# Optimization experiments

Measured on AMD Instinct MI355X. Metric: run time of the kernel, lower is better.

## Reference

```python
import jax, jax.numpy as jnp
import numpy as np

E, D, H, B = 8, 64, 512, 32768  # n_experts, state_dim, hidden width, batch
IN = D + 3  # x, t, sin(omega*t), cos(omega*t)


def setup_inputs() -> dict:
    key = jax.random.key(0)
    ks = jax.random.split(key, 12)
    s = 0.02
    return {
        "t": jax.random.uniform(ks[0], (1,), dtype=jnp.float32),
        "x": jax.random.normal(ks[1], (B, D), dtype=jnp.float32),
        "expert_weights": jax.random.uniform(ks[2], (B, E), dtype=jnp.float32),
        "omega": jnp.arange(1, E + 1, dtype=jnp.float32),  # omega_i = i+1
        "W1": jax.random.normal(ks[3], (E, H, IN), dtype=jnp.float32) * s,
        "b1": jnp.zeros((E, H), dtype=jnp.float32),
        "W2": jax.random.normal(ks[4], (E, H, H), dtype=jnp.float32) * s,
        "b2": jnp.zeros((E, H), dtype=jnp.float32),
        "W3": jax.random.normal(ks[5], (E, H, H), dtype=jnp.float32) * s,
        "b3": jnp.zeros((E, H), dtype=jnp.float32),
        "W4": jax.random.normal(ks[6], (E, D, H), dtype=jnp.float32) * s,
        "b4": jnp.zeros((E, D), dtype=jnp.float32),
    }


def reference(t, x, expert_weights, omega, W1, b1, W2, b2, W3, b3, W4, b4):
    # Dense path of ExpertODEEnsemble.forward: all experts active.
    nB = x.shape[0]
    tb = jnp.broadcast_to(t, (nB,))                       # (B,)
    wt = omega[:, None] * tb[None, :]                     # (E, B)
    # Per-expert inputs: [x, t, sin(wt), cos(wt)] -> (E, B, D+3)
    xe = jnp.broadcast_to(x[None], (E, nB, D))
    te = jnp.broadcast_to(tb[None, :, None], (E, nB, 1))
    inp = jnp.concatenate([xe, te, jnp.sin(wt)[..., None], jnp.cos(wt)[..., None]], axis=-1)
    h = jnp.tanh(jnp.einsum('ebi,ehi->ebh', inp, W1) + b1[:, None, :])
    h = jnp.tanh(jnp.einsum('ebh,egh->ebg', h, W2) + b2[:, None, :])
    h = jnp.tanh(jnp.einsum('ebh,egh->ebg', h, W3) + b3[:, None, :])
    dyn = jnp.einsum('ebh,edh->ebd', h, W4) + b4[:, None, :]   # (E, B, D)
    # Weighted combine: sum_e w[b,e] * dyn[e,b,:]
    dx_dt = jnp.einsum('be,ebd->bd', expert_weights, dyn)
    return dx_dt
```

## Files before the change

kernel.cpp:

```cpp
#include <hip/hip_runtime.h>
#include <hip/hip_bf16.h>


typedef unsigned short ushort_t;
typedef unsigned int u32;
typedef unsigned long long u64;
typedef __attribute__((ext_vector_type(8))) short short8;
typedef __attribute__((ext_vector_type(4))) float floatx4;
typedef __attribute__((ext_vector_type(16))) float floatx16;
typedef __attribute__((ext_vector_type(4))) int intx4;

#define W1A_OFF 0u
#define W2A_OFF 524288u
#define W3A_OFF 4718592u
#define W4A_OFF 8912896u
#define XB_OFF  9437184u
#define B1E_OFF 13631488u

#define X_OFF_L 135168
#define SYNC_OFF 152064
#define SMEM_SZ 152128

static __device__ __forceinline__ u32 pk2bf(float a, float b) {
  union { __hip_bfloat162 h; u32 u; } v;
  v.h = __float22bfloat162_rn(make_float2(a, b));
  return v.u;
}

static __device__ __forceinline__ float pade_tanh(float x) {
  float x2 = x * x;
  float num = __builtin_fmaf(x2, __builtin_fmaf(x2, 1.0f, 105.0f), 945.0f);
  float den = __builtin_fmaf(x2, __builtin_fmaf(x2, 15.0f, 420.0f), 945.0f);
  return x * num * __builtin_amdgcn_rcpf(den);
}

static __device__ __forceinline__ void ald16(const void* g, void* l) {
  __builtin_amdgcn_global_load_lds((__attribute__((address_space(1))) void*)g,
                                   (__attribute__((address_space(3))) void*)l,
                                   16, 0, 0);
}

static __device__ __forceinline__ floatx16 mfma32(short8 a, short8 b, floatx16 c) {
  return __builtin_amdgcn_mfma_f32_32x32x16_bf16(a, b, c, 0, 0, 0);
}

static __device__ __forceinline__ void waitge(const int* p, int tgt) {
  while (*(volatile const int*)p < tgt) __builtin_amdgcn_s_sleep(1);
  __asm__ __volatile__("" ::: "memory");
}

static __device__ __forceinline__ void bump(int* p, int lane) {
  __asm__ __volatile__("s_waitcnt lgkmcnt(0)" ::: "memory");
  if (lane == 0) atomicAdd(p, 1);
}

__global__ __launch_bounds__(256) void prep_kernel(
    const float* __restrict__ t, const float* __restrict__ x,
    const float* __restrict__ omega, const float* __restrict__ W1,
    const float* __restrict__ b1, const float* __restrict__ W2,
    const float* __restrict__ W3, const float* __restrict__ W4,
    char* __restrict__ ws) {
  int i = blockIdx.x * 256 + threadIdx.x;
  if (i < 32768) {
    int e = i >> 12, rem = i & 4095, outr = rem >> 3, kg = rem & 7;
    int lane = (outr & 31) | ((kg & 1) << 5);
    int w = outr >> 6, ol = (outr >> 5) & 1, kc = kg >> 1;
    int dest = e * 4096 + ((w * 4 + kc) * 2 + ol) * 64 + lane;
    const float* s = W1 + (e * 512 + outr) * 67 + kg * 8;
    ((intx4*)(ws + W1A_OFF))[dest] = (intx4){
        (int)pk2bf(s[0], s[1]), (int)pk2bf(s[2], s[3]),
        (int)pk2bf(s[4], s[5]), (int)pk2bf(s[6], s[7])};
    return;
  }
  i -= 32768;
  if (i < 262144) {
    int e = i >> 15, rem = i & 32767, outr = rem >> 6, kg = rem & 63;
    int lane = (outr & 31) | ((kg & 1) << 5);
    int w = outr >> 6, ol = (outr >> 5) & 1, kc = kg >> 1;
    int dest = e * 32768 + ((w * 32 + kc) * 2 + ol) * 64 + lane;
    const floatx4* s = (const floatx4*)(W2 + ((e << 9) + outr) * 512 + (kg << 3));
    floatx4 lo = s[0], hi = s[1];
    ((intx4*)(ws + W2A_OFF))[dest] = (intx4){
        (int)pk2bf(lo[0], lo[1]), (int)pk2bf(lo[2], lo[3]),
        (int)pk2bf(hi[0], hi[1]), (int)pk2bf(hi[2], hi[3])};
    return;
  }
  i -= 262144;
  if (i < 262144) {
    int e = i >> 15, rem = i & 32767, outr = rem >> 6, kg = rem & 63;
    int lane = (outr & 31) | ((kg & 1) << 5);
    int w = outr >> 6, ol = (outr >> 5) & 1, kc = kg >> 1;
    int dest = e * 32768 + ((w * 32 + kc) * 2 + ol) * 64 + lane;
    const floatx4* s = (const floatx4*)(W3 + ((e << 9) + outr) * 512 + (kg << 3));
    floatx4 lo = s[0], hi = s[1];
    ((intx4*)(ws + W3A_OFF))[dest] = (intx4){
        (int)pk2bf(lo[0], lo[1]), (int)pk2bf(lo[2], lo[3]),
        (int)pk2bf(hi[0], hi[1]), (int)pk2bf(hi[2], hi[3])};
    return;
  }
  i -= 262144;
  if (i < 32768) {
    int e = i >> 12, rem = i & 4095, outr = rem >> 6, kg = rem & 63;
    int lane = (outr & 31) | ((kg & 1) << 5);
    int o4 = outr >> 5, kc = kg >> 1;
    int dest = e * 4096 + (o4 * 32 + kc) * 64 + lane;
    const floatx4* s = (const floatx4*)(W4 + ((e << 6) + outr) * 512 + (kg << 3));
    floatx4 lo = s[0], hi = s[1];
    ((intx4*)(ws + W4A_OFF))[dest] = (intx4){
        (int)pk2bf(lo[0], lo[1]), (int)pk2bf(lo[2], lo[3]),
        (int)pk2bf(hi[0], hi[1]), (int)pk2bf(hi[2], hi[3])};
    return;
  }
  i -= 32768;
  if (i < 262144) {
    const floatx4* s = (const floatx4*)(x + i * 8);
    floatx4 lo = s[0], hi = s[1];
    ((intx4*)(ws + XB_OFF))[i] = (intx4){
        (int)pk2bf(lo[0], lo[1]), (int)pk2bf(lo[2], lo[3]),
        (int)pk2bf(hi[0], hi[1]), (int)pk2bf(hi[2], hi[3])};
    return;
  }
  i -= 262144;
  if (i < 4096) {
    float tv = t[0];
    int e = i >> 9;
    float om = omega[e];
    ((float*)(ws + B1E_OFF))[i] = b1[i] + tv * W1[i * 67 + 64]
        + sinf(om * tv) * W1[i * 67 + 65] + cosf(om * tv) * W1[i * 67 + 66];
  }
}


template <int NKC, bool ISX>
static __device__ __forceinline__ void mlp_layer(
    const char* __restrict__ bsrc, char* __restrict__ act,
    int* kcp, int* pub, int lane, int w, int q1, int r31,
    const char* __restrict__ Abase, const float* __restrict__ bias,
    int pub_tgt, int tgt_cov, int tgt_oth, int khm, bool do_epi_wait) {
  const int voff = lane * 16;
  const char* sp = Abase + w * (NKC * 2048) + voff;

  floatx16 acc[2][4];
#pragma unroll
  for (int ol = 0; ol < 2; ++ol) {
    int fe0 = w * 64 + ol * 32 + 4 * q1;
#pragma unroll
    for (int g = 0; g < 4; ++g) {
      floatx4 bv = *(const floatx4*)(bias + fe0 + 8 * g);
#pragma unroll
      for (int nt = 0; nt < 4; ++nt) {
        acc[ol][nt][4 * g + 0] = bv[0];
        acc[ol][nt][4 * g + 1] = bv[1];
        acc[ol][nt][4 * g + 2] = bv[2];
        acc[ol][nt][4 * g + 3] = bv[3];
      }
    }
  }
  short8 a0 = *(const short8*)(sp);
  short8 a1 = *(const short8*)(sp + 1024);
  sp += 2048;

  const int NG = NKC / 4;
#pragma unroll 1
  for (int g = 0; g < NG; ++g) {
    if (!ISX) waitge(pub + g, pub_tgt);
    const char* gb = bsrc + g * (4 * 4224) + voff;
    short8 b0 = *(const short8*)(gb);
    short8 b1v = *(const short8*)(gb + 1024);
    short8 b2 = *(const short8*)(gb + 2048);
    short8 b3 = *(const short8*)(gb + 3072);
#pragma unroll
    for (int j = 0; j < 4; ++j) {
      short8 an0 = *(const short8*)(sp);
      short8 an1 = *(const short8*)(sp + 1024);
      sp += 2048;
      const char* bn = gb + ((j + 1) & 3) * 4224;
      short8 bn0 = *(const short8*)(bn);
      short8 bn1 = *(const short8*)(bn + 1024);
      short8 bn2 = *(const short8*)(bn + 2048);
      short8 bn3 = *(const short8*)(bn + 3072);
      acc[0][0] = mfma32(a0, b0, acc[0][0]);
      acc[0][1] = mfma32(a0, b1v, acc[0][1]);
      acc[0][2] = mfma32(a0, b2, acc[0][2]);
      acc[0][3] = mfma32(a0, b3, acc[0][3]);
      acc[1][0] = mfma32(a1, b0, acc[1][0]);
      acc[1][1] = mfma32(a1, b1v, acc[1][1]);
      acc[1][2] = mfma32(a1, b2, acc[1][2]);
      acc[1][3] = mfma32(a1, b3, acc[1][3]);
      a0 = an0; a1 = an1;
      b0 = bn0; b1v = bn1; b2 = bn2; b3 = bn3;
    }
    bump(kcp + w, lane);
  }

  if (do_epi_wait) {
    for (int w2 = 0; w2 < 8; ++w2)
      waitge(kcp + w2, ((w2 >> 2) == khm) ? tgt_cov : tgt_oth);
  }
#pragma unroll
  for (int ol = 0; ol < 2; ++ol) {
#pragma unroll
    for (int g = 0; g < 4; ++g) {
      int ko = ol * 4 + g;
      char* base = act + (4 * w + (ko >> 1)) * 4224
                   + (((ko & 1) * 32 + r31) << 4) + q1 * 8;
#pragma unroll
      for (int nt = 0; nt < 4; ++nt) {
        float v0 = pade_tanh(acc[ol][nt][4 * g + 0]);
        float v1 = pade_tanh(acc[ol][nt][4 * g + 1]);
        float v2 = pade_tanh(acc[ol][nt][4 * g + 2]);
        float v3 = pade_tanh(acc[ol][nt][4 * g + 3]);
        u32 lo = pk2bf(v0, v1), hi = pk2bf(v2, v3);
        *(u64*)(base + nt * 1024) = ((u64)hi << 32) | lo;
      }
    }
  }
  bump(pub + w, lane);
}

extern "C" __global__ __launch_bounds__(512) void fused_kernel(
    const char* __restrict__ ws, const float* __restrict__ b2,
    const float* __restrict__ b3, const float* __restrict__ b4,
    const float* __restrict__ ew, float* __restrict__ out) {
  extern __shared__ char smem[];
  char* act = smem;
  char* xreg = smem + X_OFF_L;
  int* kcp = (int*)(smem + SYNC_OFF);
  int* pub = kcp + 8;

  const int t = threadIdx.x, lane = t & 63, w = t >> 6;
  const int q1 = lane >> 5, r31 = lane & 31;
  const int row0 = blockIdx.x << 7;
  const int voff = lane * 16;

  if (t < 16) ((int*)(smem + SYNC_OFF))[t] = 0;

  const ushort_t* xb = (const ushort_t*)(ws + XB_OFF);
#pragma unroll
  for (int s = 0; s < 2; ++s) {
    int u = w + 8 * s, v = u >> 2, nt = u & 3;
    ald16(xb + (row0 + nt * 32 + r31) * 64 + (2 * v + q1) * 8,
          xreg + v * 4224 + nt * 1024);
  }
  __syncthreads();

  const int rt = w & 3, kh = w >> 2;
  const int row_l4 = row0 + rt * 32 + r31;
  floatx16 oacc[2] = {};

  for (int e = 0; e < 8; ++e) {
    mlp_layer<4, true>(xreg, act, kcp, pub, lane, w, q1, r31,
                       ws + W1A_OFF + e * 65536,
                       (const float*)(ws + B1E_OFF) + e * 512,
                       0, 21 * e + (w & 3) - 3, 21 * e + w - 11, w >> 2, e > 0);
    mlp_layer<32, false>(act, act, kcp, pub, lane, w, q1, r31,
                         ws + W2A_OFF + e * 524288, b2 + e * 512,
                         3 * e + 1, 21 * e + w + 2, 21 * e + w + 2, 0, true);
    mlp_layer<32, false>(act, act, kcp, pub, lane, w, q1, r31,
                         ws + W3A_OFF + e * 524288, b3 + e * 512,
                         3 * e + 2, 21 * e + w + 10, 21 * e + w + 10, 0, true);

    {
      const char* spA = ws + W4A_OFF + e * 65536 + voff;
      const float sc = ew[row_l4 * 8 + e];
      floatx16 acc4[2] = {};
      int kc0 = kh * 16;
      short8 a0 = *(const short8*)(spA + kc0 * 1024);
      short8 a1 = *(const short8*)(spA + 32768 + kc0 * 1024);
#pragma unroll 1
      for (int gl = 0; gl < 4; ++gl) {
        int g = kh * 4 + gl;
        waitge(pub + g, 3 * e + 3);
        const char* gb = act + g * (4 * 4224) + rt * 1024 + voff;
        short8 b = *(const short8*)(gb);
#pragma unroll
        for (int j = 0; j < 4; ++j) {
          int kc = g * 4 + j;
          short8 an0 = *(const short8*)(spA + (kc + 1) * 1024);
          short8 an1 = *(const short8*)(spA + 32768 + (kc + 1) * 1024);
          short8 bn = *(const short8*)(gb + ((j + 1) & 3) * 4224);
          acc4[0] = mfma32(a0, b, acc4[0]);
          acc4[1] = mfma32(a1, b, acc4[1]);
          a0 = an0; a1 = an1; b = bn;
        }
        bump(kcp + w, lane);
      }
      if (kh == 0) {
        const float* bp = b4 + e * 64;
#pragma unroll
        for (int ol = 0; ol < 2; ++ol) {
          int fe0 = ol * 32 + 4 * q1;
#pragma unroll
          for (int g = 0; g < 4; ++g) {
            floatx4 bv = *(const floatx4*)(bp + fe0 + 8 * g);
            oacc[ol][4 * g + 0] += sc * (acc4[ol][4 * g + 0] + bv[0]);
            oacc[ol][4 * g + 1] += sc * (acc4[ol][4 * g + 1] + bv[1]);
            oacc[ol][4 * g + 2] += sc * (acc4[ol][4 * g + 2] + bv[2]);
            oacc[ol][4 * g + 3] += sc * (acc4[ol][4 * g + 3] + bv[3]);
          }
        }
      } else {
#pragma unroll
        for (int ol = 0; ol < 2; ++ol)
#pragma unroll
          for (int i = 0; i < 16; ++i) oacc[ol][i] += sc * acc4[ol][i];
      }
    }
  }

  __syncthreads();
  if (kh == 1) {
#pragma unroll
    for (int ol = 0; ol < 2; ++ol)
#pragma unroll
      for (int g = 0; g < 4; ++g) {
        floatx4 p = {oacc[ol][4 * g + 0], oacc[ol][4 * g + 1],
                     oacc[ol][4 * g + 2], oacc[ol][4 * g + 3]};
        *(floatx4*)(act + rt * 8192 + ol * 4096 + g * 1024 + lane * 16) = p;
      }
  }
  __syncthreads();
  if (kh == 0) {
    float* orow = out + row_l4 * 64;
#pragma unroll
    for (int ol = 0; ol < 2; ++ol)
#pragma unroll
      for (int g = 0; g < 4; ++g) {
        floatx4 p = *(const floatx4*)(act + rt * 8192 + ol * 4096 + g * 1024 + lane * 16);
        floatx4 v = {oacc[ol][4 * g + 0] + p[0], oacc[ol][4 * g + 1] + p[1],
                     oacc[ol][4 * g + 2] + p[2], oacc[ol][4 * g + 3] + p[3]};
        *(floatx4*)(orow + ol * 32 + 8 * g + 4 * q1) = v;
      }
  }
}

extern "C" void kernel_launch(void* const* d_in, const int* in_sizes, int n_in,
                              void* d_out, int out_size, void* d_ws, size_t ws_size,
                              hipStream_t stream) {
  const float* t  = (const float*)d_in[0];
  const float* x  = (const float*)d_in[1];
  const float* ew = (const float*)d_in[2];
  const float* om = (const float*)d_in[3];
  const float* W1 = (const float*)d_in[4];
  const float* b1 = (const float*)d_in[5];
  const float* W2 = (const float*)d_in[6];
  const float* b2 = (const float*)d_in[7];
  const float* W3 = (const float*)d_in[8];
  const float* b3 = (const float*)d_in[9];
  const float* W4 = (const float*)d_in[10];
  const float* b4 = (const float*)d_in[11];
  char* ws = (char*)d_ws;
  float* out = (float*)d_out;
  (void)in_sizes; (void)n_in; (void)ws_size; (void)out_size;

  static int smem_set = 0;
  if (!smem_set) {
    hipFuncSetAttribute((const void*)fused_kernel,
                        hipFuncAttributeMaxDynamicSharedMemorySize, SMEM_SZ);
    smem_set = 1;
  }
  prep_kernel<<<3344, 256, 0, stream>>>(t, x, om, W1, b1, W2, W3, W4, ws);
  fused_kernel<<<256, 512, SMEM_SZ, stream>>>(ws, b2, b3, b4, ew, out);
}
```

Measured before the change: 441.3 us.

## Rotate per-wave K-group order to stagger LDS access and flag waits

Each wave now starts its K-group loop at an offset based on its wave index and wraps around. This applies to the hidden layers and the output layer. The aim is to spread LDS bank and flag-polling contention across waves and let waves start on groups that are already published. The epilogue wait targets are recomputed as a common base plus a per-wave stagger to match the new completion order. The risk is that mismatched counter targets cause races or over-waiting.

```diff
diff --git a/kernel.cpp b/kernel.cpp
--- a/kernel.cpp
+++ b/kernel.cpp
@@ -136,9 +136,10 @@
     const char* __restrict__ bsrc, char* __restrict__ act,
     int* kcp, int* pub, int lane, int w, int q1, int r31,
     const char* __restrict__ Abase, const float* __restrict__ bias,
-    int pub_tgt, int tgt_cov, int tgt_oth, int khm, bool do_epi_wait) {
+    int pub_tgt, int epi_base, bool epi_stagger, bool do_epi_wait) {
   const int voff = lane * 16;
-  const char* sp = Abase + w * (NKC * 2048) + voff;
+  const char* Aw = Abase + w * (NKC * 2048) + voff;
+  const int NG = NKC / 4;
 
   floatx16 acc[2][4];
 #pragma unroll
@@ -156,24 +157,26 @@
       }
     }
   }
-  short8 a0 = *(const short8*)(sp);
-  short8 a1 = *(const short8*)(sp + 1024);
-  sp += 2048;
-
-  const int NG = NKC / 4;
+  const int g0 = w & (NG - 1);
+  short8 a0 = *(const short8*)(Aw + g0 * 8192);
+  short8 a1 = *(const short8*)(Aw + g0 * 8192 + 1024);
+
 #pragma unroll 1
-  for (int g = 0; g < NG; ++g) {
+  for (int gi = 0; gi < NG; ++gi) {
+    const int g = (w + gi) & (NG - 1);
     if (!ISX) waitge(pub + g, pub_tgt);
     const char* gb = bsrc + g * (4 * 4224) + voff;
     short8 b0 = *(const short8*)(gb);
     short8 b1v = *(const short8*)(gb + 1024);
     short8 b2 = *(const short8*)(gb + 2048);
     short8 b3 = *(const short8*)(gb + 3072);
+    const char* Ag = Aw + g * 8192;
+    const char* An = Aw + (((w + gi + 1) & (NG - 1)) * 8192);
 #pragma unroll
     for (int j = 0; j < 4; ++j) {
-      short8 an0 = *(const short8*)(sp);
-      short8 an1 = *(const short8*)(sp + 1024);
-      sp += 2048;
+      const char* ap = (j < 3) ? (Ag + (j + 1) * 2048) : An;
+      short8 an0 = *(const short8*)(ap);
+      short8 an1 = *(const short8*)(ap + 1024);
       const char* bn = gb + ((j + 1) & 3) * 4224;
       short8 bn0 = *(const short8*)(bn);
       short8 bn1 = *(const short8*)(bn + 1024);
@@ -194,8 +197,12 @@
   }
 
   if (do_epi_wait) {
-    for (int w2 = 0; w2 < 8; ++w2)
-      waitge(kcp + w2, ((w2 >> 2) == khm) ? tgt_cov : tgt_oth);
+    if (epi_stagger) {
+      for (int w2 = 0; w2 < 8; ++w2)
+        waitge(kcp + w2, epi_base + ((w - w2) & 7));
+    } else {
+      for (int w2 = 0; w2 < 8; ++w2) waitge(kcp + w2, epi_base);
+    }
   }
 #pragma unroll
   for (int ol = 0; ol < 2; ++ol) {
@@ -252,32 +259,33 @@
     mlp_layer<4, true>(xreg, act, kcp, pub, lane, w, q1, r31,
                        ws + W1A_OFF + e * 65536,
                        (const float*)(ws + B1E_OFF) + e * 512,
-                       0, 21 * e + (w & 3) - 3, 21 * e + w - 11, w >> 2, e > 0);
+                       0, 21 * e, false, e > 0);
     mlp_layer<32, false>(act, act, kcp, pub, lane, w, q1, r31,
                          ws + W2A_OFF + e * 524288, b2 + e * 512,
-                         3 * e + 1, 21 * e + w + 2, 21 * e + w + 2, 0, true);
+                         3 * e + 1, 21 * e + 2, true, true);
     mlp_layer<32, false>(act, act, kcp, pub, lane, w, q1, r31,
                          ws + W3A_OFF + e * 524288, b3 + e * 512,
-                         3 * e + 2, 21 * e + w + 10, 21 * e + w + 10, 0, true);
+                         3 * e + 2, 21 * e + 10, true, true);
 
     {
       const char* spA = ws + W4A_OFF + e * 65536 + voff;
       const float sc = ew[row_l4 * 8 + e];
       floatx16 acc4[2] = {};
-      int kc0 = kh * 16;
-      short8 a0 = *(const short8*)(spA + kc0 * 1024);
-      short8 a1 = *(const short8*)(spA + 32768 + kc0 * 1024);
+      const int gfirst = kh * 4 + rt;
+      short8 a0 = *(const short8*)(spA + (gfirst * 4) * 1024);
+      short8 a1 = *(const short8*)(spA + 32768 + (gfirst * 4) * 1024);
 #pragma unroll 1
       for (int gl = 0; gl < 4; ++gl) {
-        int g = kh * 4 + gl;
+        const int g = kh * 4 + ((rt + gl) & 3);
         waitge(pub + g, 3 * e + 3);
         const char* gb = act + g * (4 * 4224) + rt * 1024 + voff;
         short8 b = *(const short8*)(gb);
+        const int gnext = kh * 4 + ((rt + gl + 1) & 3);
 #pragma unroll
         for (int j = 0; j < 4; ++j) {
-          int kc = g * 4 + j;
-          short8 an0 = *(const short8*)(spA + (kc + 1) * 1024);
-          short8 an1 = *(const short8*)(spA + 32768 + (kc + 1) * 1024);
+          const int kcn = (j < 3) ? (g * 4 + j + 1) : (gnext * 4);
+          short8 an0 = *(const short8*)(spA + kcn * 1024);
+          short8 an1 = *(const short8*)(spA + 32768 + kcn * 1024);
           short8 bn = *(const short8*)(gb + ((j + 1) & 3) * 4224);
           acc4[0] = mfma32(a0, b, acc4[0]);
           acc4[1] = mfma32(a1, b, acc4[1]);
```

After: 446.5 us. Within noise of the previous version (+1.2%).
